# Performance work log

Measured on AMD Instinct MI355X. Metric: run time of the kernel, lower is better.

Reference implementation:

```python
import jax, jax.numpy as jnp
import numpy as np

D = 1024      # in_features == out_features
H = 4096      # hidden_features
E = 8         # num_experts
TOPK = 2


def setup_inputs() -> dict:
    key = jax.random.key(0)
    ks = jax.random.split(key, 6)
    x = jax.random.normal(ks[0], (8, 1024, D), dtype=jnp.float32)
    # router: torch Linear(in_features, E, bias=False); stored here as [D, E] so logits = x @ router_w
    router_w = jax.random.normal(ks[1], (D, E), dtype=jnp.float32) * (1.0 / np.sqrt(D))
    # stacked expert MLP params (torch Linear semantics: y = x @ W + b with W stored [in, out])
    w1 = jax.random.normal(ks[2], (E, D, H), dtype=jnp.float32) * (1.0 / np.sqrt(D))
    b1 = jnp.zeros((E, H), dtype=jnp.float32)
    w2 = jax.random.normal(ks[3], (E, H, D), dtype=jnp.float32) * (1.0 / np.sqrt(H))
    b2 = jnp.zeros((E, D), dtype=jnp.float32)
    return {"x": x, "router_w": router_w, "w1": w1, "b1": b1, "w2": w2, "b2": b2}


def _moe_forward(x, router_w, w1, b1, w2, b2):
    orig_shape = x.shape
    xf = x.reshape(-1, orig_shape[-1])              # [T, D]
    logits = xf @ router_w                           # [T, E]
    probs = jax.nn.softmax(logits, axis=-1)          # [T, E]
    top_p, top_i = jax.lax.top_k(probs, TOPK)        # [T, K]
    top_p = top_p / jnp.sum(top_p, axis=-1, keepdims=True)
    # combine weights: scatter normalized top-k probs into dense [T, E]
    onehot = jax.nn.one_hot(top_i, E, dtype=xf.dtype)      # [T, K, E]
    combine = jnp.einsum("tk,tke->te", top_p, onehot)      # [T, E]
    # per-expert dense MLP over all tokens, masked/weighted by combine.
    # Tokens with combine[:, e] == 0 contribute nothing (same math as sparse dispatch).
    out = jnp.zeros_like(xf)
    for e in range(E):
        h = jax.nn.gelu(xf @ w1[e] + b1[e], approximate=False)   # [T, H]
        y = h @ w2[e] + b2[e]                                     # [T, D]
        out = out + combine[:, e:e + 1] * y
    return out.reshape(orig_shape)


def reference(x, router_w, w1, b1, w2, b2):
    return _moe_forward(x, router_w, w1, b1, w2, b2)
```

## Files before the change

### kernel.cpp

```cpp
#include <hip/hip_runtime.h>
#include <hip/hip_bf16.h>


#define TT 8192
#define DD 1024
#define HH 4096
#define NE 8
#define NPAIR (TT * 2)
#define PADROWS 256
#define MBLK (NPAIR / 128 + NE)

typedef __attribute__((ext_vector_type(4))) float f32x4;
typedef __attribute__((ext_vector_type(8))) short short8;
typedef __attribute__((ext_vector_type(4))) unsigned short u16x4;

__device__ __forceinline__ unsigned short bf16rne(float f) {
  union { float f; unsigned u; } v; v.f = f;
  unsigned r = v.u + 0x7FFFu + ((v.u >> 16) & 1u);
  return (unsigned short)(r >> 16);
}

__device__ __forceinline__ float gelu_exact(float v) {
  return 0.5f * v * (1.0f + erff(v * 0.70710678118654752440f));
}

#define SWZ(r, kb) ((kb) ^ (((r) + ((r) >> 3)) & 7))

#define HDR_OFFS 16
#define HDR_TCNT 25
#define HDR_TE   32
#define HDR_TR   168

__global__ __launch_bounds__(256) void router_kernel(
    const float* __restrict__ x, const float* __restrict__ rw,
    int* __restrict__ hdr, int* __restrict__ te, float* __restrict__ tw)
{
  int t = blockIdx.x * 4 + (threadIdx.x >> 6);
  int lane = threadIdx.x & 63;
  const float* xr = x + (size_t)t * DD;
  double acc[NE];
#pragma unroll
  for (int e = 0; e < NE; ++e) acc[e] = 0.0;
  for (int i = 0; i < DD / 64; ++i) {
    int d = i * 64 + lane;
    float xv = xr[d];
    f32x4 r0 = *(const f32x4*)(rw + (size_t)d * NE);
    f32x4 r1 = *(const f32x4*)(rw + (size_t)d * NE + 4);
#pragma unroll
    for (int e = 0; e < 4; ++e) acc[e] += (double)xv * (double)r0[e];
#pragma unroll
    for (int e = 0; e < 4; ++e) acc[4 + e] += (double)xv * (double)r1[e];
  }
#pragma unroll
  for (int off = 32; off > 0; off >>= 1) {
#pragma unroll
    for (int e = 0; e < NE; ++e) acc[e] += __shfl_xor(acc[e], off);
  }
  if (lane == 0) {
    float l[NE];
#pragma unroll
    for (int e = 0; e < NE; ++e) l[e] = (float)acc[e];
    int bi = 0; float bv = l[0]; int si = -1; float sv = -3.0e38f;
#pragma unroll
    for (int e = 1; e < NE; ++e) {
      float v = l[e];
      if (v > bv) { sv = bv; si = bi; bv = v; bi = e; }
      else if (v > sv) { sv = v; si = e; }
    }
    float es = expf(sv - bv);
    float wb = 1.0f / (1.0f + es);
    float ws2 = es / (1.0f + es);
    te[2 * t] = bi; te[2 * t + 1] = si;
    tw[2 * t] = wb; tw[2 * t + 1] = ws2;
    atomicAdd(&hdr[bi], 1);
    atomicAdd(&hdr[si], 1);
  }
}

__global__ void scan_kernel(int* __restrict__ hdr) {
  if (threadIdx.x == 0) {
    int s = 0;
#pragma unroll
    for (int e = 0; e < NE; ++e) { hdr[HDR_OFFS + e] = s; s += hdr[e]; }
    hdr[HDR_OFFS + NE] = s;
    int t = 0;
    for (int e = 0; e < NE; ++e) {
      int cnt = hdr[e];
      for (int r = 0; r < cnt; r += 128) {
        hdr[HDR_TE + t] = e;
        hdr[HDR_TR + t] = r;
        ++t;
      }
    }
    hdr[HDR_TCNT] = t;
  }
  if (threadIdx.x < NE) hdr[8 + threadIdx.x] = 0;
}

__global__ __launch_bounds__(256) void assign_kernel(
    const int* __restrict__ te, const float* __restrict__ tw, int* __restrict__ hdr,
    int* __restrict__ pair_token, float* __restrict__ pair_w)
{
  int lane = threadIdx.x & 63;
  int t = blockIdx.x * 256 + threadIdx.x;
  int e0 = te[2 * t], e1 = te[2 * t + 1];
  const int* offs = hdr + HDR_OFFS;
  unsigned long long below = (1ull << lane) - 1ull;
  int slot0 = 0, slot1 = 0;
#pragma unroll
  for (int e = 0; e < NE; ++e) {
    unsigned long long m0 = __ballot(e0 == e);
    unsigned long long m1 = __ballot(e1 == e);
    int cnt = __popcll(m0) + __popcll(m1);
    int base = 0;
    if (lane == 0 && cnt) base = atomicAdd(&hdr[8 + e], cnt);
    base = __shfl(base, 0);
    int s = offs[e] + base;
    if (e0 == e) slot0 = s + __popcll(m0 & below);
    if (e1 == e) slot1 = s + __popcll(m0) + __popcll(m1 & below);
  }
  pair_token[slot0] = t; pair_w[slot0] = tw[2 * t];
  pair_token[slot1] = t; pair_w[slot1] = tw[2 * t + 1];
}

__global__ __launch_bounds__(256) void copy_kernel(
    const float* __restrict__ x, const int* __restrict__ pair_token,
    unsigned short* __restrict__ xg)
{
  int p = (blockIdx.x * 256 + threadIdx.x) >> 6;
  int lane = threadIdx.x & 63;
  int tok = pair_token[p];
  const f32x4* xr = (const f32x4*)(x + (size_t)tok * DD);
  unsigned short* d = xg + (size_t)p * DD;
#pragma unroll
  for (int i = 0; i < 4; ++i) {
    int idx = i * 64 + lane;
    f32x4 v = xr[idx];
    u16x4 b;
#pragma unroll
    for (int j = 0; j < 4; ++j) b[j] = bf16rne(v[j]);
    *(u16x4*)(d + idx * 4) = b;
  }
}

__global__ __launch_bounds__(256) void transpose_bf16_kernel(
    const float* __restrict__ W, unsigned short* __restrict__ WT, int K, int N)
{
  __shared__ unsigned short t[64][72];
  const float* src = W + (size_t)blockIdx.z * K * N;
  unsigned short* dst = WT + (size_t)blockIdx.z * N * K;
  const int K0 = blockIdx.y * 64, N0 = blockIdx.x * 64;
  const int tid = threadIdx.x;
  const int c = (tid & 15) * 4;
#pragma unroll
  for (int p = 0; p < 4; ++p) {
    int r = (tid >> 4) + p * 16;
    f32x4 v = *(const f32x4*)(src + (size_t)(K0 + r) * N + N0 + c);
    u16x4 b;
#pragma unroll
    for (int j = 0; j < 4; ++j) b[j] = bf16rne(v[j]);
    *(u16x4*)&t[r][c] = b;
  }
  __syncthreads();
  const int n = tid >> 2;
  const int k0 = (tid & 3) * 16;
  __align__(16) unsigned short tmp[16];
#pragma unroll
  for (int i = 0; i < 16; ++i) tmp[i] = t[k0 + i][n];
  unsigned short* dp = dst + (size_t)(N0 + n) * K + K0 + k0;
  *(u16x4*)(dp + 0)  = *(u16x4*)(tmp + 0);
  *(u16x4*)(dp + 4)  = *(u16x4*)(tmp + 4);
  *(u16x4*)(dp + 8)  = *(u16x4*)(tmp + 8);
  *(u16x4*)(dp + 12) = *(u16x4*)(tmp + 12);
}

template <int ACT>
__global__ __launch_bounds__(256) void moe_gemm(
    const unsigned short* __restrict__ Aall,
    const unsigned short* __restrict__ BT,
    const float* __restrict__ bias,
    const int* __restrict__ hdr,
    unsigned short* __restrict__ Hout,
    const int* __restrict__ pair_token,
    const float* __restrict__ pair_w,
    float* __restrict__ out,
    int K, int N)
{
  const int nwg = MBLK * gridDim.y;
  const int orig = blockIdx.x + MBLK * blockIdx.y;
  const int q = nwg >> 3, r = nwg & 7;
  const int xcd = orig & 7, loc = orig >> 3;
  const int wg = (xcd < r ? xcd * (q + 1) : r * (q + 1) + (xcd - r) * q) + loc;
  const int mx = wg % MBLK;
  const int ny = wg / MBLK;

  if (mx >= hdr[HDR_TCNT]) return;
  const int e = hdr[HDR_TE + mx];
  const int r0 = hdr[HDR_TR + mx];
  const int* offs = hdr + HDR_OFFS;
  const int row_base = offs[e];
  const int n_rows = offs[e + 1] - row_base;
  const int n0 = ny * 128;

  const unsigned short* A = Aall + (size_t)row_base * K;
  const unsigned short* B = BT + (size_t)e * N * K;

  __shared__ __align__(16) unsigned short Asw[128 * 64];
  __shared__ __align__(16) unsigned short Bsw[128 * 64];

  const int tid = threadIdx.x;
  const int lane = tid & 63;
  const int wv = tid >> 6;
  const int wr = wv >> 1, wc = wv & 1;

  f32x4 acc[4][4] = {};

  for (int k0 = 0; k0 < K; k0 += 64) {
    if (k0) __syncthreads();
#pragma unroll
    for (int p = 0; p < 4; ++p) {
      int s = p * 256 + tid;
      int row = s >> 3;
      int kb = SWZ(row, s & 7);
      __builtin_amdgcn_global_load_lds(
          (const __attribute__((address_space(1))) void*)(A + (size_t)(r0 + row) * K + k0 + kb * 8),
          (__attribute__((address_space(3))) void*)(Asw + s * 8), 16, 0, 0);
    }
#pragma unroll
    for (int p = 0; p < 4; ++p) {
      int s = p * 256 + tid;
      int row = s >> 3;
      int kb = SWZ(row, s & 7);
      __builtin_amdgcn_global_load_lds(
          (const __attribute__((address_space(1))) void*)(B + (size_t)(n0 + row) * K + k0 + kb * 8),
          (__attribute__((address_space(3))) void*)(Bsw + s * 8), 16, 0, 0);
    }
    __syncthreads();
#pragma unroll
    for (int s2 = 0; s2 < 2; ++s2) {
      short8 af[4], bfr[4];
      int kq = s2 * 4 + (lane >> 4);
#pragma unroll
      for (int m = 0; m < 4; ++m) {
        int row = wr * 64 + m * 16 + (lane & 15);
        af[m] = *(const short8*)(Asw + row * 64 + SWZ(row, kq) * 8);
      }
#pragma unroll
      for (int n = 0; n < 4; ++n) {
        int c = wc * 64 + n * 16 + (lane & 15);
        bfr[n] = *(const short8*)(Bsw + c * 64 + SWZ(c, kq) * 8);
      }
#pragma unroll
      for (int m = 0; m < 4; ++m)
#pragma unroll
        for (int n = 0; n < 4; ++n)
          acc[m][n] = __builtin_amdgcn_mfma_f32_16x16x32_bf16(af[m], bfr[n], acc[m][n], 0, 0, 0);
    }
  }

#pragma unroll
  for (int m = 0; m < 4; ++m) {
#pragma unroll
    for (int j = 0; j < 4; ++j) {
      int gr = r0 + wr * 64 + m * 16 + (lane >> 4) * 4 + j;
      if (gr >= n_rows) continue;
      if (ACT == 0) {
#pragma unroll
        for (int n = 0; n < 4; ++n) {
          int gc = n0 + wc * 64 + n * 16 + (lane & 15);
          float v = acc[m][n][j] + bias[e * N + gc];
          Hout[(size_t)(row_base + gr) * N + gc] = bf16rne(gelu_exact(v));
        }
      } else {
        int tok = pair_token[row_base + gr];
        float w = pair_w[row_base + gr];
#pragma unroll
        for (int n = 0; n < 4; ++n) {
          int gc = n0 + wc * 64 + n * 16 + (lane & 15);
          float v = acc[m][n][j] + bias[e * N + gc];
          atomicAdd(&out[(size_t)tok * N + gc], w * v);
        }
      }
    }
  }
}

extern "C" void kernel_launch(void* const* d_in, const int* in_sizes, int n_in,
                              void* d_out, int out_size, void* d_ws, size_t ws_size,
                              hipStream_t stream) {
  const float* x  = (const float*)d_in[0];
  const float* rw = (const float*)d_in[1];
  const float* w1 = (const float*)d_in[2];
  const float* b1 = (const float*)d_in[3];
  const float* w2 = (const float*)d_in[4];
  const float* b2 = (const float*)d_in[5];
  float* out = (float*)d_out;

  char* ws = (char*)d_ws;
  const size_t OFF_TE = 4096;
  const size_t OFF_TW = OFF_TE + (size_t)NPAIR * 4;
  const size_t OFF_PT = OFF_TW + (size_t)NPAIR * 4;
  const size_t OFF_PW = OFF_PT + (size_t)NPAIR * 4;
  const size_t OFF_XG = OFF_PW + (size_t)NPAIR * 4;
  const size_t OFF_H  = OFF_XG + (size_t)(NPAIR + PADROWS) * DD * 2;
  const size_t OFF_WT = OFF_H + (size_t)(NPAIR + PADROWS) * HH * 2;
  const size_t NEEDED = OFF_WT + (size_t)NE * DD * HH * 2;
  if (ws_size < NEEDED) return;

  int*   hdr        = (int*)ws;
  int*   te         = (int*)(ws + OFF_TE);
  float* tw         = (float*)(ws + OFF_TW);
  int*   pair_token = (int*)(ws + OFF_PT);
  float* pair_w     = (float*)(ws + OFF_PW);
  unsigned short* xg = (unsigned short*)(ws + OFF_XG);
  unsigned short* h  = (unsigned short*)(ws + OFF_H);
  unsigned short* wT = (unsigned short*)(ws + OFF_WT);

  hipMemsetAsync(d_ws, 0, 4096, stream);
  hipMemsetAsync(d_out, 0, (size_t)out_size * sizeof(float), stream);

  router_kernel<<<TT / 4, 256, 0, stream>>>(x, rw, hdr, te, tw);
  scan_kernel<<<1, 64, 0, stream>>>(hdr);
  assign_kernel<<<TT / 256, 256, 0, stream>>>(te, tw, hdr, pair_token, pair_w);
  copy_kernel<<<NPAIR / 4, 256, 0, stream>>>(x, pair_token, xg);

  transpose_bf16_kernel<<<dim3(HH / 64, DD / 64, NE), 256, 0, stream>>>(w1, wT, DD, HH);
  moe_gemm<0><<<dim3(MBLK, HH / 128), 256, 0, stream>>>(
      xg, wT, b1, hdr, h, nullptr, nullptr, nullptr, DD, HH);

  transpose_bf16_kernel<<<dim3(DD / 64, HH / 64, NE), 256, 0, stream>>>(w2, wT, HH, DD);
  moe_gemm<1><<<dim3(MBLK, DD / 128), 256, 0, stream>>>(
      h, wT, b2, hdr, nullptr, pair_token, pair_w, out, HH, DD);
}
```

Before: 827.1 us.

## Double-buffer LDS tiles in MoE GEMM and split-K the second GEMM

The MoE GEMM main loop now uses two LDS buffers, so the global-to-LDS loads for the next K tile are issued before computing the current one. Explicit vmcnt/lgkmcnt waits and barriers order the two. The second (down-projection) GEMM is also split in two along K, doubling its grid to improve occupancy, and the bias is added only by the first split. This doubles LDS use per block, which may reduce occupancy, and doubles the atomic adds into the output.

```diff
diff --git a/kernel.cpp b/kernel.cpp
--- a/kernel.cpp
+++ b/kernel.cpp
@@ -30,6 +30,12 @@
 #define HDR_TCNT 25
 #define HDR_TE   32
 #define HDR_TR   168
+
+#define VM8   asm volatile("s_waitcnt vmcnt(8)" ::: "memory")
+#define VM0   asm volatile("s_waitcnt vmcnt(0)" ::: "memory")
+#define LGKM0 asm volatile("s_waitcnt lgkmcnt(0)" ::: "memory")
+#define BAR   __builtin_amdgcn_s_barrier()
+#define SCHED0 __builtin_amdgcn_sched_barrier(0)
 
 __global__ __launch_bounds__(256) void router_kernel(
     const float* __restrict__ x, const float* __restrict__ rw,
@@ -174,7 +180,7 @@
   *(u16x4*)(dp + 12) = *(u16x4*)(tmp + 12);
 }
 
-template <int ACT>
+template <int ACT, int KSPLIT>
 __global__ __launch_bounds__(256) void moe_gemm(
     const unsigned short* __restrict__ Aall,
     const unsigned short* __restrict__ BT,
@@ -186,13 +192,16 @@
     float* __restrict__ out,
     int K, int N)
 {
+  const int NY = N >> 7;
   const int nwg = MBLK * gridDim.y;
   const int orig = blockIdx.x + MBLK * blockIdx.y;
   const int q = nwg >> 3, r = nwg & 7;
   const int xcd = orig & 7, loc = orig >> 3;
   const int wg = (xcd < r ? xcd * (q + 1) : r * (q + 1) + (xcd - r) * q) + loc;
   const int mx = wg % MBLK;
-  const int ny = wg / MBLK;
+  const int rest = wg / MBLK;
+  const int ny = rest % NY;
+  const int ks = rest / NY;
 
   if (mx >= hdr[HDR_TCNT]) return;
   const int e = hdr[HDR_TE + mx];
@@ -201,12 +210,16 @@
   const int row_base = offs[e];
   const int n_rows = offs[e + 1] - row_base;
   const int n0 = ny * 128;
+  const int kbase = ks * (K / KSPLIT);
+  const int NT = (K / KSPLIT) / 64;
 
   const unsigned short* A = Aall + (size_t)row_base * K;
   const unsigned short* B = BT + (size_t)e * N * K;
 
-  __shared__ __align__(16) unsigned short Asw[128 * 64];
-  __shared__ __align__(16) unsigned short Bsw[128 * 64];
+  __shared__ __align__(16) unsigned short Asw0[128 * 64];
+  __shared__ __align__(16) unsigned short Bsw0[128 * 64];
+  __shared__ __align__(16) unsigned short Asw1[128 * 64];
+  __shared__ __align__(16) unsigned short Bsw1[128 * 64];
 
   const int tid = threadIdx.x;
   const int lane = tid & 63;
@@ -215,8 +228,8 @@
 
   f32x4 acc[4][4] = {};
 
-  for (int k0 = 0; k0 < K; k0 += 64) {
-    if (k0) __syncthreads();
+  auto stage = [&](unsigned short* As, unsigned short* Bs, int t) {
+    const int k0 = kbase + t * 64;
 #pragma unroll
     for (int p = 0; p < 4; ++p) {
       int s = p * 256 + tid;
@@ -224,7 +237,7 @@
       int kb = SWZ(row, s & 7);
       __builtin_amdgcn_global_load_lds(
           (const __attribute__((address_space(1))) void*)(A + (size_t)(r0 + row) * K + k0 + kb * 8),
-          (__attribute__((address_space(3))) void*)(Asw + s * 8), 16, 0, 0);
+          (__attribute__((address_space(3))) void*)(As + s * 8), 16, 0, 0);
     }
 #pragma unroll
     for (int p = 0; p < 4; ++p) {
@@ -233,9 +246,11 @@
       int kb = SWZ(row, s & 7);
       __builtin_amdgcn_global_load_lds(
           (const __attribute__((address_space(1))) void*)(B + (size_t)(n0 + row) * K + k0 + kb * 8),
-          (__attribute__((address_space(3))) void*)(Bsw + s * 8), 16, 0, 0);
-    }
-    __syncthreads();
+          (__attribute__((address_space(3))) void*)(Bs + s * 8), 16, 0, 0);
+    }
+  };
+
+  auto compute = [&](const unsigned short* As, const unsigned short* Bs) {
 #pragma unroll
     for (int s2 = 0; s2 < 2; ++s2) {
       short8 af[4], bfr[4];
@@ -243,18 +258,36 @@
 #pragma unroll
       for (int m = 0; m < 4; ++m) {
         int row = wr * 64 + m * 16 + (lane & 15);
-        af[m] = *(const short8*)(Asw + row * 64 + SWZ(row, kq) * 8);
+        af[m] = *(const short8*)(As + row * 64 + SWZ(row, kq) * 8);
       }
 #pragma unroll
       for (int n = 0; n < 4; ++n) {
         int c = wc * 64 + n * 16 + (lane & 15);
-        bfr[n] = *(const short8*)(Bsw + c * 64 + SWZ(c, kq) * 8);
+        bfr[n] = *(const short8*)(Bs + c * 64 + SWZ(c, kq) * 8);
       }
 #pragma unroll
       for (int m = 0; m < 4; ++m)
 #pragma unroll
         for (int n = 0; n < 4; ++n)
           acc[m][n] = __builtin_amdgcn_mfma_f32_16x16x32_bf16(af[m], bfr[n], acc[m][n], 0, 0, 0);
+    }
+  };
+
+  stage(Asw0, Bsw0, 0);
+  for (int t = 0; t < NT; t += 2) {
+    if (t + 1 < NT) { stage(Asw1, Bsw1, t + 1); VM8; } else { VM0; }
+    SCHED0;
+    BAR;
+    compute(Asw0, Bsw0);
+    LGKM0; SCHED0;
+    BAR;
+    if (t + 1 < NT) {
+      if (t + 2 < NT) { stage(Asw0, Bsw0, t + 2); VM8; } else { VM0; }
+      SCHED0;
+      BAR;
+      compute(Asw1, Bsw1);
+      LGKM0; SCHED0;
+      BAR;
     }
   }
 
@@ -277,7 +310,7 @@
 #pragma unroll
         for (int n = 0; n < 4; ++n) {
           int gc = n0 + wc * 64 + n * 16 + (lane & 15);
-          float v = acc[m][n][j] + bias[e * N + gc];
+          float v = acc[m][n][j] + (ks == 0 ? bias[e * N + gc] : 0.0f);
           atomicAdd(&out[(size_t)tok * N + gc], w * v);
         }
       }
@@ -325,10 +358,10 @@
   copy_kernel<<<NPAIR / 4, 256, 0, stream>>>(x, pair_token, xg);
 
   transpose_bf16_kernel<<<dim3(HH / 64, DD / 64, NE), 256, 0, stream>>>(w1, wT, DD, HH);
-  moe_gemm<0><<<dim3(MBLK, HH / 128), 256, 0, stream>>>(
+  moe_gemm<0, 1><<<dim3(MBLK, HH / 128), 256, 0, stream>>>(
       xg, wT, b1, hdr, h, nullptr, nullptr, nullptr, DD, HH);
 
   transpose_bf16_kernel<<<dim3(DD / 64, HH / 64, NE), 256, 0, stream>>>(w2, wT, HH, DD);
-  moe_gemm<1><<<dim3(MBLK, DD / 128), 256, 0, stream>>>(
+  moe_gemm<1, 2><<<dim3(MBLK, (DD / 128) * 2), 256, 0, stream>>>(
       h, wT, b2, hdr, nullptr, pair_token, pair_w, out, HH, DD);
 }
```

After: 980.0 us. +18.5%, slower.

## Double-buffer LDS with K=32 tiles and explicit waitcnt in first expert GEMM

Applied to the files above, without the earlier changes.

Splits the templated MoE GEMM into two kernels and rewrites the first (x·W1 + GELU) to use two LDS buffers with 32-wide K tiles. The next tile is prefetched via global_load_lds while the current one feeds the MFMAs, and manual vmcnt/lgkmcnt waits plus scheduling barriers control the overlap. Smaller LDS per block together with launch_bounds(256,5) aims for higher occupancy. The trade-off is more barriers per unit of K and a simpler XOR swizzle that may cause more LDS bank conflicts.

```diff
diff --git a/kernel.cpp b/kernel.cpp
--- a/kernel.cpp
+++ b/kernel.cpp
@@ -25,11 +25,18 @@
 }
 
 #define SWZ(r, kb) ((kb) ^ (((r) + ((r) >> 3)) & 7))
+#define SWZ4(r, kb) ((kb) ^ ((r) & 3))
 
 #define HDR_OFFS 16
 #define HDR_TCNT 25
 #define HDR_TE   32
 #define HDR_TR   168
+
+#define VM4   asm volatile("s_waitcnt vmcnt(4)" ::: "memory")
+#define VM0   asm volatile("s_waitcnt vmcnt(0)" ::: "memory")
+#define LGKM0 asm volatile("s_waitcnt lgkmcnt(0)" ::: "memory")
+#define BAR   __builtin_amdgcn_s_barrier()
+#define SCHED0 __builtin_amdgcn_sched_barrier(0)
 
 __global__ __launch_bounds__(256) void router_kernel(
     const float* __restrict__ x, const float* __restrict__ rw,
@@ -174,19 +181,15 @@
   *(u16x4*)(dp + 12) = *(u16x4*)(tmp + 12);
 }
 
-template <int ACT>
-__global__ __launch_bounds__(256) void moe_gemm(
+__global__ __launch_bounds__(256, 5) void moe_gemm1(
     const unsigned short* __restrict__ Aall,
     const unsigned short* __restrict__ BT,
     const float* __restrict__ bias,
     const int* __restrict__ hdr,
-    unsigned short* __restrict__ Hout,
-    const int* __restrict__ pair_token,
-    const float* __restrict__ pair_w,
-    float* __restrict__ out,
-    int K, int N)
-{
-  const int nwg = MBLK * gridDim.y;
+    unsigned short* __restrict__ Hout)
+{
+  const int K = DD, N = HH;
+  const int nwg = MBLK * (N >> 7);
   const int orig = blockIdx.x + MBLK * blockIdx.y;
   const int q = nwg >> 3, r = nwg & 7;
   const int xcd = orig & 7, loc = orig >> 3;
@@ -205,6 +208,124 @@
   const unsigned short* A = Aall + (size_t)row_base * K;
   const unsigned short* B = BT + (size_t)e * N * K;
 
+  __shared__ __align__(16) unsigned short Asw0[128 * 32];
+  __shared__ __align__(16) unsigned short Bsw0[128 * 32];
+  __shared__ __align__(16) unsigned short Asw1[128 * 32];
+  __shared__ __align__(16) unsigned short Bsw1[128 * 32];
+
+  const int tid = threadIdx.x;
+  const int lane = tid & 63;
+  const int wv = tid >> 6;
+  const int wr = wv >> 1, wc = wv & 1;
+
+  f32x4 acc[4][4] = {};
+  const int NT = K / 32;
+
+  auto stage = [&](unsigned short* As, unsigned short* Bs, int t) {
+    const int k0 = t * 32;
+#pragma unroll
+    for (int p = 0; p < 2; ++p) {
+      int s = p * 256 + tid;
+      int row = s >> 2;
+      int kb = SWZ4(row, s & 3);
+      __builtin_amdgcn_global_load_lds(
+          (const __attribute__((address_space(1))) void*)(A + (size_t)(r0 + row) * K + k0 + kb * 8),
+          (__attribute__((address_space(3))) void*)(As + s * 8), 16, 0, 0);
+    }
+#pragma unroll
+    for (int p = 0; p < 2; ++p) {
+      int s = p * 256 + tid;
+      int row = s >> 2;
+      int kb = SWZ4(row, s & 3);
+      __builtin_amdgcn_global_load_lds(
+          (const __attribute__((address_space(1))) void*)(B + (size_t)(n0 + row) * K + k0 + kb * 8),
+          (__attribute__((address_space(3))) void*)(Bs + s * 8), 16, 0, 0);
+    }
+  };
+
+  auto compute = [&](const unsigned short* As, const unsigned short* Bs) {
+    short8 af[4], bfr[4];
+    int kq = lane >> 4;
+#pragma unroll
+    for (int m = 0; m < 4; ++m) {
+      int row = wr * 64 + m * 16 + (lane & 15);
+      af[m] = *(const short8*)(As + row * 32 + SWZ4(row, kq) * 8);
+    }
+#pragma unroll
+    for (int n = 0; n < 4; ++n) {
+      int c = wc * 64 + n * 16 + (lane & 15);
+      bfr[n] = *(const short8*)(Bs + c * 32 + SWZ4(c, kq) * 8);
+    }
+#pragma unroll
+    for (int m = 0; m < 4; ++m)
+#pragma unroll
+      for (int n = 0; n < 4; ++n)
+        acc[m][n] = __builtin_amdgcn_mfma_f32_16x16x32_bf16(af[m], bfr[n], acc[m][n], 0, 0, 0);
+  };
+
+  stage(Asw0, Bsw0, 0);
+  for (int t = 0; t < NT; t += 2) {
+    if (t + 1 < NT) { stage(Asw1, Bsw1, t + 1); VM4; } else { VM0; }
+    SCHED0;
+    BAR;
+    compute(Asw0, Bsw0);
+    LGKM0; SCHED0;
+    BAR;
+    if (t + 1 < NT) {
+      if (t + 2 < NT) { stage(Asw0, Bsw0, t + 2); VM4; } else { VM0; }
+      SCHED0;
+      BAR;
+      compute(Asw1, Bsw1);
+      LGKM0; SCHED0;
+      BAR;
+    }
+  }
+
+#pragma unroll
+  for (int m = 0; m < 4; ++m) {
+#pragma unroll
+    for (int j = 0; j < 4; ++j) {
+      int gr = r0 + wr * 64 + m * 16 + (lane >> 4) * 4 + j;
+      if (gr >= n_rows) continue;
+#pragma unroll
+      for (int n = 0; n < 4; ++n) {
+        int gc = n0 + wc * 64 + n * 16 + (lane & 15);
+        float v = acc[m][n][j] + bias[e * N + gc];
+        Hout[(size_t)(row_base + gr) * N + gc] = bf16rne(gelu_exact(v));
+      }
+    }
+  }
+}
+
+__global__ __launch_bounds__(256) void moe_gemm2(
+    const unsigned short* __restrict__ Aall,
+    const unsigned short* __restrict__ BT,
+    const float* __restrict__ bias,
+    const int* __restrict__ hdr,
+    const int* __restrict__ pair_token,
+    const float* __restrict__ pair_w,
+    float* __restrict__ out)
+{
+  const int K = HH, N = DD;
+  const int nwg = MBLK * (N >> 7);
+  const int orig = blockIdx.x + MBLK * blockIdx.y;
+  const int q = nwg >> 3, r = nwg & 7;
+  const int xcd = orig & 7, loc = orig >> 3;
+  const int wg = (xcd < r ? xcd * (q + 1) : r * (q + 1) + (xcd - r) * q) + loc;
+  const int mx = wg % MBLK;
+  const int ny = wg / MBLK;
+
+  if (mx >= hdr[HDR_TCNT]) return;
+  const int e = hdr[HDR_TE + mx];
+  const int r0 = hdr[HDR_TR + mx];
+  const int* offs = hdr + HDR_OFFS;
+  const int row_base = offs[e];
+  const int n_rows = offs[e + 1] - row_base;
+  const int n0 = ny * 128;
+
+  const unsigned short* A = Aall + (size_t)row_base * K;
+  const unsigned short* B = BT + (size_t)e * N * K;
+
   __shared__ __align__(16) unsigned short Asw[128 * 64];
   __shared__ __align__(16) unsigned short Bsw[128 * 64];
 
@@ -264,22 +385,13 @@
     for (int j = 0; j < 4; ++j) {
       int gr = r0 + wr * 64 + m * 16 + (lane >> 4) * 4 + j;
       if (gr >= n_rows) continue;
-      if (ACT == 0) {
-#pragma unroll
-        for (int n = 0; n < 4; ++n) {
-          int gc = n0 + wc * 64 + n * 16 + (lane & 15);
-          float v = acc[m][n][j] + bias[e * N + gc];
-          Hout[(size_t)(row_base + gr) * N + gc] = bf16rne(gelu_exact(v));
-        }
-      } else {
-        int tok = pair_token[row_base + gr];
-        float w = pair_w[row_base + gr];
-#pragma unroll
-        for (int n = 0; n < 4; ++n) {
-          int gc = n0 + wc * 64 + n * 16 + (lane & 15);
-          float v = acc[m][n][j] + bias[e * N + gc];
-          atomicAdd(&out[(size_t)tok * N + gc], w * v);
-        }
+      int tok = pair_token[row_base + gr];
+      float w = pair_w[row_base + gr];
+#pragma unroll
+      for (int n = 0; n < 4; ++n) {
+        int gc = n0 + wc * 64 + n * 16 + (lane & 15);
+        float v = acc[m][n][j] + bias[e * N + gc];
+        atomicAdd(&out[(size_t)tok * N + gc], w * v);
       }
     }
   }
@@ -325,10 +437,9 @@
   copy_kernel<<<NPAIR / 4, 256, 0, stream>>>(x, pair_token, xg);
 
   transpose_bf16_kernel<<<dim3(HH / 64, DD / 64, NE), 256, 0, stream>>>(w1, wT, DD, HH);
-  moe_gemm<0><<<dim3(MBLK, HH / 128), 256, 0, stream>>>(
-      xg, wT, b1, hdr, h, nullptr, nullptr, nullptr, DD, HH);
+  moe_gemm1<<<dim3(MBLK, HH / 128), 256, 0, stream>>>(xg, wT, b1, hdr, h);
 
   transpose_bf16_kernel<<<dim3(DD / 64, HH / 64, NE), 256, 0, stream>>>(w2, wT, HH, DD);
-  moe_gemm<1><<<dim3(MBLK, DD / 128), 256, 0, stream>>>(
-      h, wT, b2, hdr, nullptr, pair_token, pair_w, out, HH, DD);
-}
+  moe_gemm2<<<dim3(MBLK, DD / 128), 256, 0, stream>>>(
+      h, wT, b2, hdr, pair_token, pair_w, out);
+}
```

Result: slower. 948.7 us (+14.7%).
